# Kernel optimization log

Measured on AMD Instinct MI355X. Metric: run time of the kernel, lower is better.

Reference implementation:

```python
import jax, jax.numpy as jnp
import numpy as np

NN_SIZE = 10  # __init__ default nn_size


def setup_inputs() -> dict:
    key = jax.random.key(0)
    k1, k2 = jax.random.split(key)
    B, N, C = 8, 4096, 3
    xyz1 = jax.random.normal(k1, (B, N, C), dtype=jnp.float32)
    # xyz2 is a small deformation of xyz1 (realistic: deformed shape, same topology)
    xyz2 = xyz1 + 0.05 * jax.random.normal(k2, (B, N, C), dtype=jnp.float32)
    return {"xyz1": xyz1, "xyz2": xyz2}


def _knn_idx(pts, k):
    # brute-force squared-euclidean KNN of pts to itself; pts: (B,N,3) -> idx (B,N,k)
    sq = jnp.sum(pts * pts, axis=-1)                             # (B,N)
    d = sq[:, :, None] - 2.0 * jnp.einsum('bnc,bmc->bnm', pts, pts) + sq[:, None, :]
    _, idx = jax.lax.top_k(-d, k)                                # smallest distances
    return idx


def _point_to_plane(xyz, idx, k):
    # gather neighbors, center, PCA normal from 10x3 SVD, signed point-to-plane dist
    B, N, C = xyz.shape
    grouped = jax.vmap(lambda p, i: p[i])(xyz, idx)              # (B,N,k,3)
    center = jnp.mean(grouped, axis=2, keepdims=True)            # (B,N,1,3)
    local = (grouped - center).reshape(B * N, k, C)              # (B*N,k,3)
    _, _, vh = jnp.linalg.svd(local, full_matrices=False)        # vh: (B*N,3,3)
    # torch V[:, :, -1] == row -1 of Vh: singular vector of smallest singular value
    normals = jax.lax.stop_gradient(vh[:, -1, :].reshape(B, N, C))
    return jnp.sum((xyz - center[:, :, 0, :]) * normals, axis=-1)  # (B,N)


def reference(xyz1, xyz2):
    idx = _knn_idx(xyz1, NN_SIZE)
    ptof1 = _point_to_plane(xyz1, idx, NN_SIZE)
    ptof2 = _point_to_plane(xyz2, idx, NN_SIZE)
    mse = lambda a, b: jnp.mean((a - b) ** 2)
    loss = mse(jnp.abs(ptof1), jnp.abs(ptof2))
    bent = jnp.maximum(ptof2 - ptof1, 0.0)
    loss = loss + 5.0 * mse(bent, jnp.zeros_like(bent))
    return loss
```

## Files before the change

kernel.cpp:

```cpp
#include <hip/hip_runtime.h>
#include <math.h>

#define BB   8
#define NN   4096
#define KK   10
#define TPB  256
#define NPTS (BB * NN)

#define GPP  16
#define PPB  (TPB / GPP)
#define BPBK (NN / PPB)
#define KNBLK (BB * BPBK)
#define TILE 512
#define CAP  48

#define SVDBLK 256
#define SBLK   256

#define LARTG_OLD 0
#define EPSV  5.9604644775390625e-8
#define UNFLV 1.1754943508222875e-38
#define TOLV (10.0 * EPSV)

static __device__ __forceinline__ double lapy2d(double x, double y) {
  double xa = fabs(x), ya = fabs(y);
  double w = fmax(xa, ya), z = fmin(xa, ya);
  if (z == 0.0) return w;
  double q = z / w;
  return w * sqrt(1.0 + q * q);
}

static __device__ __forceinline__ void lartg(double f, double g,
                                             double &c, double &s, double &r) {
#if LARTG_OLD
  if (g == 0.0) { c = 1.0; s = 0.0; r = f; }
  else if (f == 0.0) { c = 0.0; s = 1.0; r = g; }
  else {
    double d = sqrt(f * f + g * g);
    c = f / d; s = g / d; r = d;
    if (fabs(f) > fabs(g) && c < 0.0) { c = -c; s = -s; r = -r; }
  }
#else
  if (g == 0.0) { c = 1.0; s = 0.0; r = f; }
  else if (f == 0.0) { c = 0.0; s = copysign(1.0, g); r = fabs(g); }
  else {
    double d = sqrt(f * f + g * g);
    c = fabs(f) / d;
    r = copysign(d, f);
    s = g / r;
  }
#endif
}

static __device__ void las2(double f, double g, double h, double &ssmin, double &ssmax) {
  double fa = fabs(f), ga = fabs(g), ha = fabs(h);
  double fhmn = fmin(fa, ha), fhmx = fmax(fa, ha);
  if (fhmn == 0.0) {
    ssmin = 0.0;
    if (fhmx == 0.0) ssmax = ga;
    else {
      double mn = fmin(fhmx, ga), mx = fmax(fhmx, ga);
      double rr = mn / mx;
      ssmax = mx * sqrt(1.0 + rr * rr);
    }
  } else {
    if (ga < fhmx) {
      double as_ = 1.0 + fhmn / fhmx;
      double at  = (fhmx - fhmn) / fhmx;
      double au  = (ga / fhmx); au = au * au;
      double c   = 2.0 / (sqrt(as_ * as_ + au) + sqrt(at * at + au));
      ssmin = fhmn * c;
      ssmax = fhmx / c;
    } else {
      double au = fhmx / ga;
      if (au == 0.0) { ssmin = (fhmn * fhmx) / ga; ssmax = ga; }
      else {
        double as_ = 1.0 + fhmn / fhmx;
        double at  = (fhmx - fhmn) / fhmx;
        double t1 = as_ * au, t2 = at * au;
        double c = 1.0 / (sqrt(1.0 + t1 * t1) + sqrt(1.0 + t2 * t2));
        ssmin = (fhmn * c) * au; ssmin = ssmin + ssmin;
        ssmax = ga / (c + c);
      }
    }
  }
}

static __device__ void lasv2(double f, double g, double h,
                             double &ssmin, double &ssmax,
                             double &snr, double &csr, double &snl, double &csl) {
  double ft = f, fa = fabs(f), ht = h, ha = fabs(h);
  int pmax = 1;
  bool swp = (ha > fa);
  if (swp) { pmax = 3; double t = ft; ft = ht; ht = t; t = fa; fa = ha; ha = t; }
  double gt = g, ga = fabs(g);
  double clt = 0, crt = 0, slt = 0, srt = 0;
  if (ga == 0.0) {
    ssmin = ha; ssmax = fa;
    clt = 1.0; crt = 1.0; slt = 0.0; srt = 0.0;
  } else {
    bool gasmal = true;
    if (ga > fa) {
      pmax = 2;
      if ((fa / ga) < EPSV) {
        gasmal = false;
        ssmax = ga;
        if (ha > 1.0) ssmin = fa / (ga / ha);
        else          ssmin = (fa / ga) * ha;
        clt = 1.0; slt = ht / gt; srt = 1.0; crt = ft / gt;
      }
    }
    if (gasmal) {
      double dd = fa - ha, l;
      if (dd == fa) l = 1.0; else l = dd / fa;
      double mv = gt / ft;
      double t = 2.0 - l;
      double mm = mv * mv, tt = t * t;
      double s = sqrt(tt + mm);
      double r = (l == 0.0) ? fabs(mv) : sqrt(l * l + mm);
      double a = 0.5 * (s + r);
      ssmin = ha / a;
      ssmax = fa * a;
      if (mm == 0.0) {
        if (l == 0.0) t = copysign(2.0, ft) * copysign(1.0, gt);
        else          t = gt / copysign(dd, ft) + mv / t;
      } else {
        t = (mv / (s + t) + mv / (r + l)) * (1.0 + a);
      }
      double lq = sqrt(t * t + 4.0);
      crt = 2.0 / lq;
      srt = t / lq;
      clt = (crt + srt * mv) / a;
      slt = (ht / ft) * srt / a;
    }
  }
  if (swp) { csl = srt; snl = crt; csr = slt; snr = clt; }
  else     { csl = clt; snl = slt; csr = crt; snr = srt; }
  double tsign = 1.0;
  if (pmax == 1) tsign = copysign(1.0, csr) * copysign(1.0, csl) * copysign(1.0, f);
  if (pmax == 2) tsign = copysign(1.0, snr) * copysign(1.0, csl) * copysign(1.0, g);
  if (pmax == 3) tsign = copysign(1.0, snr) * copysign(1.0, snl) * copysign(1.0, h);
  ssmax = copysign(ssmax, tsign);
  ssmin = copysign(ssmin, tsign * copysign(1.0, f) * copysign(1.0, h));
}

static __device__ __forceinline__ void rot_rows(double vt[3][3], int lo, double c, double s) {
  if (c != 1.0 || s != 0.0) {
    for (int k = 0; k < 3; ++k) {
      double tp = vt[lo + 1][k];
      vt[lo + 1][k] = c * tp - s * vt[lo][k];
      vt[lo][k]     = s * tp + c * vt[lo][k];
    }
  }
}

static __device__ void bdsqr3(double d[3], double e[2], double vt[3][3]) {
  const double tol = TOLV;
  double sminoa = fabs(d[0]);
  if (sminoa != 0.0) {
    double mu = sminoa;
    mu = fabs(d[1]) * (mu / (mu + fabs(e[0])));
    sminoa = fmin(sminoa, mu);
    if (sminoa != 0.0) {
      mu = fabs(d[2]) * (mu / (mu + fabs(e[1])));
      sminoa = fmin(sminoa, mu);
    }
  }
  sminoa /= sqrt(3.0);
  double thresh = fmax(tol * sminoa, 54.0 * UNFLV);
  int m = 3, oldll = -1, oldm = -1, idir = 0;
  double sminl = 0.0;
  for (int guard = 0; guard < 500 && m > 1; ++guard) {
    double smax = fabs(d[m - 1]);
    int ll = 0;
    bool split = false;
    for (int lll = 1; lll <= m - 1; ++lll) {
      int l = m - lll;
      double abss = fabs(d[l - 1]);
      double abse = fabs(e[l - 1]);
      if (abse <= thresh) { ll = l; split = true; break; }
      smax = fmax(smax, fmax(abss, abse));
    }
    if (split) {
      e[ll - 1] = 0.0;
      if (ll == m - 1) { m = m - 1; continue; }
      ll = ll + 1;
    } else ll = 1;
    if (ll == m - 1) {
      double sigmn, sigmx, sinr, cosr, sinl, cosl;
      lasv2(d[m - 2], e[m - 2], d[m - 1], sigmn, sigmx, sinr, cosr, sinl, cosl);
      d[m - 2] = sigmx; e[m - 2] = 0.0; d[m - 1] = sigmn;
      for (int k = 0; k < 3; ++k) {
        double x = vt[m - 2][k], y = vt[m - 1][k];
        vt[m - 2][k] = cosr * x + sinr * y;
        vt[m - 1][k] = cosr * y - sinr * x;
      }
      m -= 2;
      continue;
    }
    if (ll > oldm || m < oldll)
      idir = (fabs(d[ll - 1]) >= fabs(d[m - 1])) ? 1 : 2;
    bool deflated = false;
    if (idir == 1) {
      if (fabs(e[m - 2]) <= tol * fabs(d[m - 1])) { e[m - 2] = 0.0; continue; }
      double mu = fabs(d[ll - 1]);
      sminl = mu;
      for (int lll = ll; lll <= m - 1; ++lll) {
        if (fabs(e[lll - 1]) <= tol * mu) { e[lll - 1] = 0.0; deflated = true; break; }
        mu = fabs(d[lll]) * (mu / (mu + fabs(e[lll - 1])));
        sminl = fmin(sminl, mu);
      }
    } else {
      if (fabs(e[ll - 1]) <= tol * fabs(d[ll - 1])) { e[ll - 1] = 0.0; continue; }
      double mu = fabs(d[m - 1]);
      sminl = mu;
      for (int lll = m - 1; lll >= ll; --lll) {
        if (fabs(e[lll - 1]) <= tol * mu) { e[lll - 1] = 0.0; deflated = true; break; }
        mu = fabs(d[lll - 1]) * (mu / (mu + fabs(e[lll - 1])));
        sminl = fmin(sminl, mu);
      }
    }
    if (deflated) continue;
    oldll = ll; oldm = m;
    double shift = 0.0, rdum = 0.0;
    if (!(3.0 * tol * (sminl / smax) <= fmax(EPSV, 0.01 * tol))) {
      double sll;
      if (idir == 1) { sll = fabs(d[ll - 1]); las2(d[m - 2], e[m - 2], d[m - 1], shift, rdum); }
      else           { sll = fabs(d[m - 1]); las2(d[ll - 1], e[ll - 1], d[ll], shift, rdum); }
      if (sll > 0.0 && (shift / sll) * (shift / sll) < EPSV) shift = 0.0;
    }
    double csv[2], snv[2];
    if (shift == 0.0) {
      if (idir == 1) {
        double cs = 1.0, oldcs = 1.0, sn = 0.0, oldsn = 0.0, r = 0.0;
        for (int i = ll; i <= m - 1; ++i) {
          lartg(d[i - 1] * cs, e[i - 1], cs, sn, r);
          if (i > ll) e[i - 2] = oldsn * r;
          lartg(oldcs * r, d[i] * sn, oldcs, oldsn, d[i - 1]);
          csv[i - ll] = cs; snv[i - ll] = sn;
        }
        double h = d[m - 1] * cs;
        d[m - 1] = h * oldcs;
        e[m - 2] = h * oldsn;
        for (int j = 0; j <= m - ll - 1; ++j) rot_rows(vt, ll - 1 + j, csv[j], snv[j]);
        if (fabs(e[m - 2]) <= thresh) e[m - 2] = 0.0;
      } else {
        double cs = 1.0, oldcs = 1.0, sn = 0.0, oldsn = 0.0, r = 0.0;
        for (int i = m; i >= ll + 1; --i) {
          lartg(d[i - 1] * cs, e[i - 2], cs, sn, r);
          if (i < m) e[i - 1] = oldsn * r;
          lartg(oldcs * r, d[i - 2] * sn, oldcs, oldsn, d[i - 1]);
          csv[i - ll - 1] = oldcs; snv[i - ll - 1] = -oldsn;
        }
        double h = d[ll - 1] * cs;
        d[ll - 1] = h * oldcs;
        e[ll - 1] = h * oldsn;
        for (int j = m - ll - 1; j >= 0; --j) rot_rows(vt, ll - 1 + j, csv[j], snv[j]);
        if (fabs(e[ll - 1]) <= thresh) e[ll - 1] = 0.0;
      }
    } else {
      if (idir == 1) {
        double f = (fabs(d[ll - 1]) - shift) * (copysign(1.0, d[ll - 1]) + shift / d[ll - 1]);
        double g = e[ll - 1], cosr, sinr, cosl, sinl, r;
        for (int i = ll; i <= m - 1; ++i) {
          lartg(f, g, cosr, sinr, r);
          if (i > ll) e[i - 2] = r;
          f = cosr * d[i - 1] + sinr * e[i - 1];
          e[i - 1] = cosr * e[i - 1] - sinr * d[i - 1];
          g = sinr * d[i];
          d[i] = cosr * d[i];
          lartg(f, g, cosl, sinl, r);
          d[i - 1] = r;
          f = cosl * e[i - 1] + sinl * d[i];
          d[i] = cosl * d[i] - sinl * e[i - 1];
          if (i < m - 1) { g = sinl * e[i]; e[i] = cosl * e[i]; }
          csv[i - ll] = cosr; snv[i - ll] = sinr;
        }
        e[m - 2] = f;
        for (int j = 0; j <= m - ll - 1; ++j) rot_rows(vt, ll - 1 + j, csv[j], snv[j]);
        if (fabs(e[m - 2]) <= thresh) e[m - 2] = 0.0;
      } else {
        double f = (fabs(d[m - 1]) - shift) * (copysign(1.0, d[m - 1]) + shift / d[m - 1]);
        double g = e[m - 2], cosr, sinr, cosl, sinl, r;
        for (int i = m; i >= ll + 1; --i) {
          lartg(f, g, cosr, sinr, r);
          if (i < m) e[i - 1] = r;
          f = cosr * d[i - 1] + sinr * e[i - 2];
          e[i - 2] = cosr * e[i - 2] - sinr * d[i - 1];
          g = sinr * d[i - 2];
          d[i - 2] = cosr * d[i - 2];
          lartg(f, g, cosl, sinl, r);
          d[i - 1] = r;
          f = cosl * e[i - 2] + sinl * d[i - 2];
          d[i - 2] = cosl * d[i - 2] - sinl * e[i - 2];
          if (i > ll + 1) { g = sinl * e[i - 3]; e[i - 3] = cosl * e[i - 3]; }
          csv[i - ll - 1] = cosr; snv[i - ll - 1] = sinr;
        }
        e[ll - 1] = f;
        for (int j = m - ll - 1; j >= 0; --j) rot_rows(vt, ll - 1 + j, csv[j], snv[j]);
        if (fabs(e[ll - 1]) <= thresh) e[ll - 1] = 0.0;
      }
    }
  }
  for (int i = 0; i < 3; ++i)
    if (d[i] < 0.0) { d[i] = -d[i]; for (int k = 0; k < 3; ++k) vt[i][k] = -vt[i][k]; }
}

static __device__ void lapack_normal(double A[KK][3], double &nx, double &ny, double &nz) {
#pragma unroll
  for (int i = 0; i < 3; ++i) {
    double ss = 0.0;
#pragma unroll
    for (int j = i + 1; j < KK; ++j) ss += A[j][i] * A[j][i];
    double xnorm = sqrt(ss);
    if (xnorm != 0.0) {
      double alpha = A[i][i];
      double beta = -copysign(lapy2d(alpha, xnorm), alpha);
      double tau = (beta - alpha) / beta;
      double sc = 1.0 / (alpha - beta);
#pragma unroll
      for (int j = i + 1; j < KK; ++j) A[j][i] *= sc;
      A[i][i] = beta;
#pragma unroll
      for (int c = i + 1; c < 3; ++c) {
        double w = A[i][c];
#pragma unroll
        for (int j = i + 1; j < KK; ++j) w += A[j][i] * A[j][c];
        w *= tau;
        A[i][c] -= w;
#pragma unroll
        for (int j = i + 1; j < KK; ++j) A[j][c] -= w * A[j][i];
      }
    }
  }
  double r11 = A[0][0], r12 = A[0][1], r13 = A[0][2];
  double r22 = A[1][1], r23 = A[1][2], r33 = A[2][2];
  double d[3], e[2];
  double taup1 = 0.0, v3 = 0.0;
  d[0] = r11;
  double a22 = r22, a23 = r23, a32 = 0.0, a33 = r33;
  if (r13 != 0.0) {
    double betap = -copysign(lapy2d(r12, r13), r12);
    taup1 = (betap - r12) / betap;
    v3 = r13 / (r12 - betap);
    e[0] = betap;
    double w2 = (a22 + a23 * v3) * taup1;
    a22 -= w2; a23 -= w2 * v3;
    double w3 = (a33 * v3) * taup1;
    a32 = -w3; a33 -= w3 * v3;
  } else {
    e[0] = r12;
  }
  if (a32 != 0.0) {
    double beta2 = -copysign(lapy2d(a22, a32), a22);
    double tq = (beta2 - a22) / beta2;
    double v2 = a32 / (a22 - beta2);
    d[1] = beta2;
    double w = (a23 + v2 * a33) * tq;
    a23 -= w; a33 -= w * v2;
  } else d[1] = a22;
  e[1] = a23;
  d[2] = a33;
  double vt[3][3] = {{1,0,0},{0,1,0},{0,0,1}};
  bdsqr3(d, e, vt);
  int im = 0;
  if (d[1] < d[im]) im = 1;
  if (d[2] < d[im]) im = 2;
  double w1 = vt[im][0], w2 = vt[im][1], w3 = vt[im][2];
  double sdot = (w2 + w3 * v3) * taup1;
  w2 -= sdot; w3 -= sdot * v3;
  double inv = 1.0 / sqrt(w1 * w1 + w2 * w2 + w3 * w3);
  nx = w1 * inv; ny = w2 * inv; nz = w3 * inv;
}

#define INS2(Kp) { bool lt_ = x < Kp; unsigned long long old_ = Kp; Kp = lt_ ? x : Kp; x = lt_ ? old_ : x; }
#define CSWAPU(U,V) { if (V < U) { unsigned long long t_ = U; U = V; V = t_; } }
#define CSWAPFD(U,V) { float mx_ = fmaxf(U, V); V = fminf(U, V); U = mx_; }

static __device__ __forceinline__ float score_s(float qx, float qy, float qz, float qw,
                                                float xi, float yi, float zi) {
  return fmaf(xi, qx, fmaf(yi, qy, fmaf(zi, qz, qw)));
}
static __device__ __forceinline__ float sqnorm(float x, float y, float z) {
  return __fadd_rn(__fadd_rn(__fmul_rn(x, x), __fmul_rn(y, y)), __fmul_rn(z, z));
}
static __device__ __forceinline__ unsigned long long s_key(float s, int idx) {
  unsigned u = __float_as_uint(s);
  u = (u & 0x80000000u) ? ~u : (u | 0x80000000u);
  return ((unsigned long long)(~u) << 32) | (unsigned)idx;
}

__global__ __launch_bounds__(TPB, 1)
void lfl_knn(const float* __restrict__ xyz1, int* __restrict__ idxbuf) {
  __shared__ float4 tile[TILE];
  __shared__ unsigned long long gbuf[PPB][CAP];
  __shared__ unsigned int gcnt[PPB];
  const int t    = threadIdx.x;
  const int b    = blockIdx.x / BPBK;
  const int pb   = blockIdx.x % BPBK;
  const int g    = t >> 4;
  const int sub  = t & 15;
  const int i    = pb * PPB + g;
  const float* base = xyz1 + (size_t)b * NN * 3;

  const float xi = base[3 * i], yi = base[3 * i + 1], zi = base[3 * i + 2];

  float b0 = -INFINITY, b1 = -INFINITY, b2 = -INFINITY, b3 = -INFINITY,
        b4 = -INFINITY, b5 = -INFINITY, b6 = -INFINITY, b7 = -INFINITY;

  for (int t0 = 0; t0 < NN; t0 += TILE) {
    for (int p = t; p < TILE; p += TPB) {
      int j = t0 + p;
      float x = base[3 * j], y = base[3 * j + 1], z = base[3 * j + 2];
      tile[p] = make_float4(x, y, z, __fmul_rn(-0.5f, sqnorm(x, y, z)));
    }
    __syncthreads();
    for (int k = 0; k < TILE / GPP; k += 8) {
      float4 q0 = tile[sub + (k + 0) * GPP];
      float4 q1 = tile[sub + (k + 1) * GPP];
      float4 q2 = tile[sub + (k + 2) * GPP];
      float4 q3 = tile[sub + (k + 3) * GPP];
      float4 q4 = tile[sub + (k + 4) * GPP];
      float4 q5 = tile[sub + (k + 5) * GPP];
      float4 q6 = tile[sub + (k + 6) * GPP];
      float4 q7 = tile[sub + (k + 7) * GPP];
      b0 = fmaxf(b0, score_s(q0.x, q0.y, q0.z, q0.w, xi, yi, zi));
      b1 = fmaxf(b1, score_s(q1.x, q1.y, q1.z, q1.w, xi, yi, zi));
      b2 = fmaxf(b2, score_s(q2.x, q2.y, q2.z, q2.w, xi, yi, zi));
      b3 = fmaxf(b3, score_s(q3.x, q3.y, q3.z, q3.w, xi, yi, zi));
      b4 = fmaxf(b4, score_s(q4.x, q4.y, q4.z, q4.w, xi, yi, zi));
      b5 = fmaxf(b5, score_s(q5.x, q5.y, q5.z, q5.w, xi, yi, zi));
      b6 = fmaxf(b6, score_s(q6.x, q6.y, q6.z, q6.w, xi, yi, zi));
      b7 = fmaxf(b7, score_s(q7.x, q7.y, q7.z, q7.w, xi, yi, zi));
    }
    __syncthreads();
  }
  CSWAPFD(b0, b1) CSWAPFD(b2, b3) CSWAPFD(b4, b5) CSWAPFD(b6, b7)
  CSWAPFD(b0, b2) CSWAPFD(b1, b3) CSWAPFD(b4, b6) CSWAPFD(b5, b7)
  CSWAPFD(b1, b2) CSWAPFD(b5, b6)
  CSWAPFD(b0, b4) CSWAPFD(b1, b5) CSWAPFD(b2, b6) CSWAPFD(b3, b7)
  CSWAPFD(b2, b4) CSWAPFD(b3, b5)
  CSWAPFD(b1, b2) CSWAPFD(b3, b4) CSWAPFD(b5, b6)

  float thr;
  {
    float m = b0;
#pragma unroll
    for (int r = 0; r < KK; ++r) {
      m = b0;
      m = fmaxf(m, __shfl_xor(m, 1));
      m = fmaxf(m, __shfl_xor(m, 2));
      m = fmaxf(m, __shfl_xor(m, 4));
      m = fmaxf(m, __shfl_xor(m, 8));
      if (b0 == m) { b0 = b1; b1 = b2; b2 = b3; b3 = b4; b4 = b5; b5 = b6; b6 = b7; b7 = -INFINITY; }
    }
    thr = m;
  }

  if (sub == 0) gcnt[g] = 0;
  __syncthreads();

  for (int t0 = 0; t0 < NN; t0 += TILE) {
    for (int p = t; p < TILE; p += TPB) {
      int j = t0 + p;
      float x = base[3 * j], y = base[3 * j + 1], z = base[3 * j + 2];
      tile[p] = make_float4(x, y, z, __fmul_rn(-0.5f, sqnorm(x, y, z)));
    }
    __syncthreads();
#pragma unroll 8
    for (int c = sub; c < TILE; c += GPP) {
      float4 q = tile[c];
      float s = score_s(q.x, q.y, q.z, q.w, xi, yi, zi);
      if (s >= thr) {
        unsigned long long key = s_key(s, t0 + c);
        unsigned pos = atomicAdd(&gcnt[g], 1u);
        if (pos < (unsigned)CAP) gbuf[g][pos] = key;
      }
    }
    __syncthreads();
  }

  const unsigned cnt = gcnt[g];
  const int gid = b * NN + i;

  if (cnt <= (unsigned)CAP) {
    unsigned long long e0 = (sub      < (int)cnt) ? gbuf[g][sub]      : ~0ULL;
    unsigned long long e1 = (sub + 16 < (int)cnt) ? gbuf[g][sub + 16] : ~0ULL;
    unsigned long long e2 = (sub + 32 < (int)cnt) ? gbuf[g][sub + 32] : ~0ULL;
    CSWAPU(e0, e1) CSWAPU(e1, e2) CSWAPU(e0, e1)
#pragma unroll
    for (int r = 0; r < KK; ++r) {
      unsigned long long m = e0, o;
      o = __shfl_xor(m, 1); m = (o < m) ? o : m;
      o = __shfl_xor(m, 2); m = (o < m) ? o : m;
      o = __shfl_xor(m, 4); m = (o < m) ? o : m;
      o = __shfl_xor(m, 8); m = (o < m) ? o : m;
      if (e0 == m) { e0 = e1; e1 = e2; e2 = ~0ULL; }
      if (sub == (r & 15)) idxbuf[gid * KK + r] = (int)(unsigned)(m & 0xFFFFFFFFULL);
    }
  } else {
    unsigned long long k0 = ~0ULL, k1 = ~0ULL, k2 = ~0ULL, k3 = ~0ULL, k4 = ~0ULL,
                       k5 = ~0ULL, k6 = ~0ULL, k7 = ~0ULL, k8 = ~0ULL, k9 = ~0ULL;
    for (int c = sub; c < NN; c += GPP) {
      float x = base[3 * c], y = base[3 * c + 1], z = base[3 * c + 2];
      float s = score_s(x, y, z, __fmul_rn(-0.5f, sqnorm(x, y, z)), xi, yi, zi);
      unsigned long long key = s_key(s, c);
      if (key < k9) {
        unsigned long long x2 = key;
        { unsigned long long &x = x2;
          INS2(k0) INS2(k1) INS2(k2) INS2(k3) INS2(k4)
          INS2(k5) INS2(k6) INS2(k7) INS2(k8) INS2(k9) }
      }
    }
#pragma unroll
    for (int r = 0; r < KK; ++r) {
      unsigned long long m = k0, o;
      o = __shfl_xor(m, 1); m = (o < m) ? o : m;
      o = __shfl_xor(m, 2); m = (o < m) ? o : m;
      o = __shfl_xor(m, 4); m = (o < m) ? o : m;
      o = __shfl_xor(m, 8); m = (o < m) ? o : m;
      if (k0 == m) { k0=k1;k1=k2;k2=k3;k3=k4;k4=k5;k5=k6;k6=k7;k7=k8;k8=k9;k9=~0ULL; }
      if (sub == (r & 15)) idxbuf[gid * KK + r] = (int)(unsigned)(m & 0xFFFFFFFFULL);
    }
  }
}

__global__ __launch_bounds__(TPB, 1)
void lfl_svd(const float* __restrict__ xyz1, const float* __restrict__ xyz2,
             const int* __restrict__ idxbuf, double* __restrict__ partials) {
  __shared__ double pv[TPB];
  __shared__ double red1[128], red2[128];
  const int t = threadIdx.x;
  const int half = t >> 7;
  const int lt = t & 127;
  const int pid = blockIdx.x * 128 + lt;
  const int b = pid / NN, i = pid % NN;
  const float* basep = (half == 0) ? (xyz1 + (size_t)b * NN * 3)
                                   : (xyz2 + (size_t)b * NN * 3);
  double p;
  {
    double A[KK][3];
    double cx = 0, cy = 0, cz = 0;
#pragma unroll
    for (int s = 0; s < KK; ++s) {
      int j = idxbuf[pid * KK + s];
      j = ((unsigned)j < (unsigned)NN) ? j : 0;
      A[s][0] = (double)basep[3 * j];
      A[s][1] = (double)basep[3 * j + 1];
      A[s][2] = (double)basep[3 * j + 2];
      cx += A[s][0]; cy += A[s][1]; cz += A[s][2];
    }
    cx *= 0.1; cy *= 0.1; cz *= 0.1;
#pragma unroll
    for (int s = 0; s < KK; ++s) { A[s][0] -= cx; A[s][1] -= cy; A[s][2] -= cz; }
    double nx, ny, nz;
    lapack_normal(A, nx, ny, nz);
    p = ((double)basep[3 * i] - cx) * nx + ((double)basep[3 * i + 1] - cy) * ny +
        ((double)basep[3 * i + 2] - cz) * nz;
  }
  pv[t] = p;
  __syncthreads();

  if (t < 128) {
    double p1 = pv[t], p2 = pv[t + 128];
    double da = fabs(p1) - fabs(p2);
    double df = p2 - p1;
    double bent = df > 0.0 ? df : 0.0;
    red1[t] = da * da;
    red2[t] = bent * bent;
  }
  __syncthreads();
  for (int s = 64; s > 0; s >>= 1) {
    if (t < s) { red1[t] += red1[t + s]; red2[t] += red2[t + s]; }
    __syncthreads();
  }
  if (t == 0) {
    partials[2 * blockIdx.x]     = red1[0];
    partials[2 * blockIdx.x + 1] = red2[0];
  }
}

__global__ __launch_bounds__(TPB)
void lfl_final(const double* __restrict__ partials, float* __restrict__ out) {
  __shared__ double r1[TPB], r2[TPB];
  const int t = threadIdx.x;
  r1[t] = partials[2 * t];
  r2[t] = partials[2 * t + 1];
  __syncthreads();
  for (int s = TPB / 2; s > 0; s >>= 1) {
    if (t < s) { r1[t] += r1[t + s]; r2[t] += r2[t + s]; }
    __syncthreads();
  }
  if (t == 0) out[0] = (float)((r1[0] + 5.0 * r2[0]) / (double)NPTS);
}

extern "C" void kernel_launch(void* const* d_in, const int* in_sizes, int n_in,
                              void* d_out, int out_size, void* d_ws, size_t ws_size,
                              hipStream_t stream) {
  const float* xyz1 = (const float*)d_in[0];
  const float* xyz2 = (const float*)d_in[1];
  float* out = (float*)d_out;
  double* partials = (double*)d_ws;
  int* idxbuf = (int*)((char*)d_ws + 4096);

  lfl_knn<<<KNBLK, TPB, 0, stream>>>(xyz1, idxbuf);
  lfl_svd<<<SVDBLK, TPB, 0, stream>>>(xyz1, xyz2, idxbuf, partials);
  lfl_final<<<1, TPB, 0, stream>>>(partials, out);
}
```

Measured before the change: 103.2 us.

## Register-block four query points per 16-lane group in the KNN kernel

Each 16-thread group in the KNN kernel now handles four query points instead of one. Each shared-memory tile element is loaded once and scored against four register-held queries, cutting LDS traffic per score and raising arithmetic intensity. Per-lane running maxima per point drop from 8 to 4 to contain register pressure. That makes the pruning threshold looser, so more candidates may pass, overflow the 48-slot buffer and fall into the slow brute-force path. The grid also shrinks fourfold, and shared candidate buffers grow, which reduces parallelism.

```diff
diff --git a/kernel.cpp b/kernel.cpp
--- a/kernel.cpp
+++ b/kernel.cpp
@@ -8,7 +8,9 @@
 #define NPTS (BB * NN)
 
 #define GPP  16
-#define PPB  (TPB / GPP)
+#define PPG  4
+#define NGRP (TPB / GPP)
+#define PPB  (NGRP * PPG)
 #define BPBK (NN / PPB)
 #define KNBLK (BB * BPBK)
 #define TILE 512
@@ -400,127 +402,133 @@
   const int pb   = blockIdx.x % BPBK;
   const int g    = t >> 4;
   const int sub  = t & 15;
-  const int i    = pb * PPB + g;
+  const int ib   = pb * PPB + g * PPG;
   const float* base = xyz1 + (size_t)b * NN * 3;
 
-  const float xi = base[3 * i], yi = base[3 * i + 1], zi = base[3 * i + 2];
-
-  float b0 = -INFINITY, b1 = -INFINITY, b2 = -INFINITY, b3 = -INFINITY,
-        b4 = -INFINITY, b5 = -INFINITY, b6 = -INFINITY, b7 = -INFINITY;
+  float px[PPG], py[PPG], pz[PPG];
+#pragma unroll
+  for (int p = 0; p < PPG; ++p) {
+    px[p] = base[3 * (ib + p)];
+    py[p] = base[3 * (ib + p) + 1];
+    pz[p] = base[3 * (ib + p) + 2];
+  }
+
+  float acc[PPG][4];
+#pragma unroll
+  for (int p = 0; p < PPG; ++p)
+#pragma unroll
+    for (int r = 0; r < 4; ++r) acc[p][r] = -INFINITY;
 
   for (int t0 = 0; t0 < NN; t0 += TILE) {
-    for (int p = t; p < TILE; p += TPB) {
-      int j = t0 + p;
+    for (int pp = t; pp < TILE; pp += TPB) {
+      int j = t0 + pp;
       float x = base[3 * j], y = base[3 * j + 1], z = base[3 * j + 2];
-      tile[p] = make_float4(x, y, z, __fmul_rn(-0.5f, sqnorm(x, y, z)));
+      tile[pp] = make_float4(x, y, z, __fmul_rn(-0.5f, sqnorm(x, y, z)));
     }
     __syncthreads();
-    for (int k = 0; k < TILE / GPP; k += 8) {
+    for (int k = 0; k < TILE / GPP; k += 4) {
       float4 q0 = tile[sub + (k + 0) * GPP];
       float4 q1 = tile[sub + (k + 1) * GPP];
       float4 q2 = tile[sub + (k + 2) * GPP];
       float4 q3 = tile[sub + (k + 3) * GPP];
-      float4 q4 = tile[sub + (k + 4) * GPP];
-      float4 q5 = tile[sub + (k + 5) * GPP];
-      float4 q6 = tile[sub + (k + 6) * GPP];
-      float4 q7 = tile[sub + (k + 7) * GPP];
-      b0 = fmaxf(b0, score_s(q0.x, q0.y, q0.z, q0.w, xi, yi, zi));
-      b1 = fmaxf(b1, score_s(q1.x, q1.y, q1.z, q1.w, xi, yi, zi));
-      b2 = fmaxf(b2, score_s(q2.x, q2.y, q2.z, q2.w, xi, yi, zi));
-      b3 = fmaxf(b3, score_s(q3.x, q3.y, q3.z, q3.w, xi, yi, zi));
-      b4 = fmaxf(b4, score_s(q4.x, q4.y, q4.z, q4.w, xi, yi, zi));
-      b5 = fmaxf(b5, score_s(q5.x, q5.y, q5.z, q5.w, xi, yi, zi));
-      b6 = fmaxf(b6, score_s(q6.x, q6.y, q6.z, q6.w, xi, yi, zi));
-      b7 = fmaxf(b7, score_s(q7.x, q7.y, q7.z, q7.w, xi, yi, zi));
+#pragma unroll
+      for (int p = 0; p < PPG; ++p) {
+        acc[p][0] = fmaxf(acc[p][0], score_s(q0.x, q0.y, q0.z, q0.w, px[p], py[p], pz[p]));
+        acc[p][1] = fmaxf(acc[p][1], score_s(q1.x, q1.y, q1.z, q1.w, px[p], py[p], pz[p]));
+        acc[p][2] = fmaxf(acc[p][2], score_s(q2.x, q2.y, q2.z, q2.w, px[p], py[p], pz[p]));
+        acc[p][3] = fmaxf(acc[p][3], score_s(q3.x, q3.y, q3.z, q3.w, px[p], py[p], pz[p]));
+      }
     }
     __syncthreads();
   }
-  CSWAPFD(b0, b1) CSWAPFD(b2, b3) CSWAPFD(b4, b5) CSWAPFD(b6, b7)
-  CSWAPFD(b0, b2) CSWAPFD(b1, b3) CSWAPFD(b4, b6) CSWAPFD(b5, b7)
-  CSWAPFD(b1, b2) CSWAPFD(b5, b6)
-  CSWAPFD(b0, b4) CSWAPFD(b1, b5) CSWAPFD(b2, b6) CSWAPFD(b3, b7)
-  CSWAPFD(b2, b4) CSWAPFD(b3, b5)
-  CSWAPFD(b1, b2) CSWAPFD(b3, b4) CSWAPFD(b5, b6)
-
-  float thr;
-  {
-    float m = b0;
+
+  float thrp[PPG];
+#pragma unroll
+  for (int p = 0; p < PPG; ++p) {
+    float c0 = acc[p][0], c1 = acc[p][1], c2 = acc[p][2], c3 = acc[p][3];
+    CSWAPFD(c0, c1) CSWAPFD(c2, c3) CSWAPFD(c0, c2) CSWAPFD(c1, c3) CSWAPFD(c1, c2)
+    float m = c0;
 #pragma unroll
     for (int r = 0; r < KK; ++r) {
-      m = b0;
+      m = c0;
       m = fmaxf(m, __shfl_xor(m, 1));
       m = fmaxf(m, __shfl_xor(m, 2));
       m = fmaxf(m, __shfl_xor(m, 4));
       m = fmaxf(m, __shfl_xor(m, 8));
-      if (b0 == m) { b0 = b1; b1 = b2; b2 = b3; b3 = b4; b4 = b5; b5 = b6; b6 = b7; b7 = -INFINITY; }
-    }
-    thr = m;
-  }
-
-  if (sub == 0) gcnt[g] = 0;
+      if (c0 == m) { c0 = c1; c1 = c2; c2 = c3; c3 = -INFINITY; }
+    }
+    thrp[p] = m;
+  }
+
+  if (t < PPB) gcnt[t] = 0;
   __syncthreads();
 
   for (int t0 = 0; t0 < NN; t0 += TILE) {
-    for (int p = t; p < TILE; p += TPB) {
-      int j = t0 + p;
+    for (int pp = t; pp < TILE; pp += TPB) {
+      int j = t0 + pp;
       float x = base[3 * j], y = base[3 * j + 1], z = base[3 * j + 2];
-      tile[p] = make_float4(x, y, z, __fmul_rn(-0.5f, sqnorm(x, y, z)));
+      tile[pp] = make_float4(x, y, z, __fmul_rn(-0.5f, sqnorm(x, y, z)));
     }
     __syncthreads();
-#pragma unroll 8
+#pragma unroll 4
     for (int c = sub; c < TILE; c += GPP) {
       float4 q = tile[c];
-      float s = score_s(q.x, q.y, q.z, q.w, xi, yi, zi);
-      if (s >= thr) {
-        unsigned long long key = s_key(s, t0 + c);
-        unsigned pos = atomicAdd(&gcnt[g], 1u);
-        if (pos < (unsigned)CAP) gbuf[g][pos] = key;
+#pragma unroll
+      for (int p = 0; p < PPG; ++p) {
+        float s = score_s(q.x, q.y, q.z, q.w, px[p], py[p], pz[p]);
+        if (s >= thrp[p]) {
+          unsigned long long key = s_key(s, t0 + c);
+          unsigned pos = atomicAdd(&gcnt[g * PPG + p], 1u);
+          if (pos < (unsigned)CAP) gbuf[g * PPG + p][pos] = key;
+        }
       }
     }
     __syncthreads();
   }
 
-  const unsigned cnt = gcnt[g];
-  const int gid = b * NN + i;
-
-  if (cnt <= (unsigned)CAP) {
-    unsigned long long e0 = (sub      < (int)cnt) ? gbuf[g][sub]      : ~0ULL;
-    unsigned long long e1 = (sub + 16 < (int)cnt) ? gbuf[g][sub + 16] : ~0ULL;
-    unsigned long long e2 = (sub + 32 < (int)cnt) ? gbuf[g][sub + 32] : ~0ULL;
-    CSWAPU(e0, e1) CSWAPU(e1, e2) CSWAPU(e0, e1)
-#pragma unroll
-    for (int r = 0; r < KK; ++r) {
-      unsigned long long m = e0, o;
-      o = __shfl_xor(m, 1); m = (o < m) ? o : m;
-      o = __shfl_xor(m, 2); m = (o < m) ? o : m;
-      o = __shfl_xor(m, 4); m = (o < m) ? o : m;
-      o = __shfl_xor(m, 8); m = (o < m) ? o : m;
-      if (e0 == m) { e0 = e1; e1 = e2; e2 = ~0ULL; }
-      if (sub == (r & 15)) idxbuf[gid * KK + r] = (int)(unsigned)(m & 0xFFFFFFFFULL);
-    }
-  } else {
-    unsigned long long k0 = ~0ULL, k1 = ~0ULL, k2 = ~0ULL, k3 = ~0ULL, k4 = ~0ULL,
-                       k5 = ~0ULL, k6 = ~0ULL, k7 = ~0ULL, k8 = ~0ULL, k9 = ~0ULL;
-    for (int c = sub; c < NN; c += GPP) {
-      float x = base[3 * c], y = base[3 * c + 1], z = base[3 * c + 2];
-      float s = score_s(x, y, z, __fmul_rn(-0.5f, sqnorm(x, y, z)), xi, yi, zi);
-      unsigned long long key = s_key(s, c);
-      if (key < k9) {
-        unsigned long long x2 = key;
-        { unsigned long long &x = x2;
-          INS2(k0) INS2(k1) INS2(k2) INS2(k3) INS2(k4)
-          INS2(k5) INS2(k6) INS2(k7) INS2(k8) INS2(k9) }
-      }
-    }
-#pragma unroll
-    for (int r = 0; r < KK; ++r) {
-      unsigned long long m = k0, o;
-      o = __shfl_xor(m, 1); m = (o < m) ? o : m;
-      o = __shfl_xor(m, 2); m = (o < m) ? o : m;
-      o = __shfl_xor(m, 4); m = (o < m) ? o : m;
-      o = __shfl_xor(m, 8); m = (o < m) ? o : m;
-      if (k0 == m) { k0=k1;k1=k2;k2=k3;k3=k4;k4=k5;k5=k6;k6=k7;k7=k8;k8=k9;k9=~0ULL; }
-      if (sub == (r & 15)) idxbuf[gid * KK + r] = (int)(unsigned)(m & 0xFFFFFFFFULL);
+  const int gidbase = b * NN + ib;
+  for (int p = 0; p < PPG; ++p) {
+    const int pt = g * PPG + p;
+    const unsigned cnt = gcnt[pt];
+    if (cnt <= (unsigned)CAP) {
+      unsigned long long e0 = (sub      < (int)cnt) ? gbuf[pt][sub]      : ~0ULL;
+      unsigned long long e1 = (sub + 16 < (int)cnt) ? gbuf[pt][sub + 16] : ~0ULL;
+      unsigned long long e2 = (sub + 32 < (int)cnt) ? gbuf[pt][sub + 32] : ~0ULL;
+      CSWAPU(e0, e1) CSWAPU(e1, e2) CSWAPU(e0, e1)
+#pragma unroll
+      for (int r = 0; r < KK; ++r) {
+        unsigned long long m = e0, o;
+        o = __shfl_xor(m, 1); m = (o < m) ? o : m;
+        o = __shfl_xor(m, 2); m = (o < m) ? o : m;
+        o = __shfl_xor(m, 4); m = (o < m) ? o : m;
+        o = __shfl_xor(m, 8); m = (o < m) ? o : m;
+        if (e0 == m) { e0 = e1; e1 = e2; e2 = ~0ULL; }
+        if (sub == (r & 15)) idxbuf[(gidbase + p) * KK + r] = (int)(unsigned)(m & 0xFFFFFFFFULL);
+      }
+    } else {
+      unsigned long long k0 = ~0ULL, k1 = ~0ULL, k2 = ~0ULL, k3 = ~0ULL, k4 = ~0ULL,
+                         k5 = ~0ULL, k6 = ~0ULL, k7 = ~0ULL, k8 = ~0ULL, k9 = ~0ULL;
+      for (int c = sub; c < NN; c += GPP) {
+        float x = base[3 * c], y = base[3 * c + 1], z = base[3 * c + 2];
+        float s = score_s(x, y, z, __fmul_rn(-0.5f, sqnorm(x, y, z)), px[p], py[p], pz[p]);
+        unsigned long long key = s_key(s, c);
+        if (key < k9) {
+          unsigned long long x2 = key;
+          { unsigned long long &x = x2;
+            INS2(k0) INS2(k1) INS2(k2) INS2(k3) INS2(k4)
+            INS2(k5) INS2(k6) INS2(k7) INS2(k8) INS2(k9) }
+        }
+      }
+#pragma unroll
+      for (int r = 0; r < KK; ++r) {
+        unsigned long long m = k0, o;
+        o = __shfl_xor(m, 1); m = (o < m) ? o : m;
+        o = __shfl_xor(m, 2); m = (o < m) ? o : m;
+        o = __shfl_xor(m, 4); m = (o < m) ? o : m;
+        o = __shfl_xor(m, 8); m = (o < m) ? o : m;
+        if (k0 == m) { k0=k1;k1=k2;k2=k3;k3=k4;k4=k5;k5=k6;k6=k7;k7=k8;k8=k9;k9=~0ULL; }
+        if (sub == (r & 15)) idxbuf[(gidbase + p) * KK + r] = (int)(unsigned)(m & 0xFFFFFFFFULL);
+      }
     }
   }
 }
```

Result: slower. 126.5 us (+22.6%).
